# Kernel optimization log

Measured on AMD Instinct MI355X. Metric: run time of the kernel, lower is better.

Reference implementation:

```python
import math
import jax, jax.numpy as jnp
import numpy as np

NQ = 10      # n_qubits
NB = 4       # n_blocks (angle encoding layers)
VD = 6       # vqc_depth (hardware-efficient layers)
LAT = 128    # latent_dim
NOBS = 9     # n_qubits - k_local + 1 sliding 2-local groups
DIM = 2 ** NQ


def sin_embed(t, dim):
    half = dim // 2
    freqs = jnp.exp(-math.log(10000.0) * jnp.arange(half, dtype=jnp.float32) / half)
    args = t[:, None] * freqs[None, :]
    return jnp.concatenate([jnp.cos(args), jnp.sin(args)], axis=-1)


def apply_ry(psi, theta, q):
    # psi: [B, 2^NQ] complex; theta: scalar or [B]
    B = psi.shape[0]
    p = psi.reshape(B, 2 ** q, 2, 2 ** (NQ - 1 - q))
    th = jnp.broadcast_to(theta, (B,))
    c = jnp.cos(th / 2)[:, None, None].astype(psi.dtype)
    s = jnp.sin(th / 2)[:, None, None].astype(psi.dtype)
    p0, p1 = p[:, :, 0, :], p[:, :, 1, :]
    return jnp.stack([c * p0 - s * p1, s * p0 + c * p1], axis=2).reshape(B, -1)


def apply_cnot(psi, ctrl, tgt):
    B = psi.shape[0]
    pt = psi.reshape((B,) + (2,) * NQ)
    p0 = jax.lax.index_in_dim(pt, 0, axis=ctrl + 1, keepdims=True)
    p1 = jnp.flip(jax.lax.index_in_dim(pt, 1, axis=ctrl + 1, keepdims=True), axis=tgt + 1)
    return jnp.concatenate([p0, p1], axis=ctrl + 1).reshape(B, -1)


def run_circuit(enc, var_params):
    B = enc.shape[0]
    psi = jnp.zeros((B, DIM), dtype=jnp.complex64).at[:, 0].set(1.0)
    # angle encoding: RY data re-uploading blocks with CNOT ladders between blocks
    for layer in range(NB):
        for q in range(NQ):
            psi = apply_ry(psi, enc[:, layer * NQ + q], q)
        if layer < NB - 1:
            for q in range(0, NQ - 1, 2):
                psi = apply_cnot(psi, q, q + 1)
            for q in range(1, NQ - 1, 2):
                psi = apply_cnot(psi, q, q + 1)
    # hardware-efficient variational layers
    for ly in range(VD):
        for q in range(NQ):
            psi = apply_ry(psi, var_params[ly, q], q)
        for q in range(0, NQ - 1, 2):
            psi = apply_cnot(psi, q, q + 1)
        for q in range(1, NQ - 1, 2):
            psi = apply_cnot(psi, q, q + 1)
    return psi


def build_H(A_p, B_p, D_p):
    # create_Hermitian: lower-tri (row-major) = A + iB; h[i-1,i-1] = D[i]; H = h + h^dagger
    r, c = np.tril_indices(4, -1)  # order matches count+j loop: (1,0),(2,0),(2,1),(3,0),(3,1),(3,2)
    L = jnp.zeros((NOBS, 4, 4), dtype=jnp.complex64)
    L = L.at[:, r, c].set(A_p.astype(jnp.complex64) + 1j * B_p.astype(jnp.complex64))
    d = 2.0 * jnp.concatenate([D_p[:, 1:4], jnp.zeros((NOBS, 1), dtype=D_p.dtype)], axis=1)
    H = L + jnp.conj(jnp.swapaxes(L, 1, 2))
    H = H + jax.vmap(jnp.diag)(d).astype(jnp.complex64)
    return H


def expvals(psi, H):
    B = psi.shape[0]
    outs = []
    for s in range(NOBS):  # sliding window [s, s+1]
        pg = psi.reshape(B, 2 ** s, 4, 2 ** (NQ - s - 2))
        outs.append(jnp.einsum('balr,lk,bakr->b', jnp.conj(pg), H[s], pg).real)
    return jnp.stack(outs, axis=-1)


def setup_inputs() -> dict:
    ks = jax.random.split(jax.random.key(0), 12)
    B = 2048
    return {
        'z_t': jax.random.normal(ks[0], (B, LAT), dtype=jnp.float32),
        't': jax.random.uniform(ks[1], (B,), dtype=jnp.float32),
        'W1': 0.05 * jax.random.normal(ks[2], (2 * LAT, 256), dtype=jnp.float32),
        'b1': jnp.zeros((256,), dtype=jnp.float32),
        'W2': 0.05 * jax.random.normal(ks[3], (256, NB * NQ), dtype=jnp.float32),
        'b2': jnp.zeros((NB * NQ,), dtype=jnp.float32),
        'var_params': 0.01 * jax.random.normal(ks[4], (VD, NQ), dtype=jnp.float32),
        'A_p': 2.0 * jax.random.normal(ks[5], (NOBS, 6), dtype=jnp.float32),
        'B_p': 2.0 * jax.random.normal(ks[6], (NOBS, 6), dtype=jnp.float32),
        'D_p': 2.0 * jax.random.normal(ks[7], (NOBS, 4), dtype=jnp.float32),
        'W3': 0.05 * jax.random.normal(ks[8], (NOBS, 256), dtype=jnp.float32),
        'b3': jnp.zeros((256,), dtype=jnp.float32),
        'W4': 0.05 * jax.random.normal(ks[9], (256, LAT), dtype=jnp.float32),
        'b4': jnp.zeros((LAT,), dtype=jnp.float32),
    }


def reference(z_t, t, W1, b1, W2, b2, var_params, A_p, B_p, D_p, W3, b3, W4, b4):
    x = jnp.concatenate([z_t, sin_embed(t, LAT)], axis=-1)   # [B, 2*LAT]
    h = jax.nn.silu(x @ W1 + b1)
    enc = h @ W2 + b2                                         # [B, NB*NQ]
    psi = run_circuit(enc, var_params)                        # [B, 2^NQ]
    obs = expvals(psi, build_H(A_p, B_p, D_p))                # [B, NOBS]
    return jax.nn.silu(obs @ W3 + b3) @ W4 + b4               # [B, LAT]
```

## Files before the change

### kernel.cpp

```cpp
#include <hip/hip_runtime.h>
#include <math.h>

#define NQ   10
#define DIM  1024
#define NOBS 9
#define LATD 128

__device__ __forceinline__ float silu_f(float x) { return x / (1.f + expf(-x)); }

template<int CTRL>
__device__ __forceinline__ float dpp_perm(float x) {
  return __int_as_float(__builtin_amdgcn_update_dpp(0, __float_as_int(x), CTRL, 0xF, 0xF, true));
}


__device__ __forceinline__ float wave_reduce_sum(float x) {
#pragma unroll
  for (int m = 32; m >= 1; m >>= 1) x += __shfl_xor(x, m, 64);
  return x;
}

template<int M>
__device__ __forceinline__ void ry_reg(float v[16], float c, float s) {
#pragma unroll
  for (int r = 0; r < 16; ++r) {
    if ((r & M) == 0) {
      float p0 = v[r], p1 = v[r | M];
      v[r]     = c * p0 - s * p1;
      v[r | M] = s * p0 + c * p1;
    }
  }
}

template<int MASK>
__device__ __forceinline__ void ry_lane(float v[16], float c, float s, int lane) {
  float sp = (lane & MASK) ? s : -s;
#pragma unroll
  for (int r = 0; r < 16; ++r) {
    float p = __shfl_xor(v[r], MASK, 64);
    v[r] = c * v[r] + sp * p;
  }
}

template<int CTRL, int MASK>
__device__ __forceinline__ void ry_lane_dpp(float v[16], float c, float s, int lane) {
  float sp = (lane & MASK) ? s : -s;
#pragma unroll
  for (int r = 0; r < 16; ++r) {
    float p = dpp_perm<CTRL>(v[r]);
    v[r] = c * v[r] + sp * p;
  }
}

__device__ __forceinline__ void apply_rys(float v[16], int lane,
                                          const float* __restrict__ cc,
                                          const float* __restrict__ ss) {
  ry_reg<8>(v, cc[0], ss[0]);
  ry_reg<4>(v, cc[1], ss[1]);
  ry_reg<2>(v, cc[2], ss[2]);
  ry_reg<1>(v, cc[3], ss[3]);
  ry_lane<32>(v, cc[4], ss[4], lane);
  ry_lane<16>(v, cc[5], ss[5], lane);
  ry_lane_dpp<0x128, 8>(v, cc[6], ss[6], lane);
  ry_lane<4>(v, cc[7], ss[7], lane);
  ry_lane_dpp<0x4E, 2>(v, cc[8], ss[8], lane);
  ry_lane_dpp<0xB1, 1>(v, cc[9], ss[9], lane);
}

__device__ __forceinline__ void cnot_ladder(float v[16], int lane) {
  float t;
  t=v[8];  v[8]=v[12];  v[12]=t;
  t=v[9];  v[9]=v[13];  v[13]=t;
  t=v[10]; v[10]=v[14]; v[14]=t;
  t=v[11]; v[11]=v[15]; v[15]=t;
  t=v[2];  v[2]=v[3];   v[3]=t;
  t=v[6];  v[6]=v[7];   v[7]=t;
  t=v[10]; v[10]=v[11]; v[11]=t;
  t=v[14]; v[14]=v[15]; v[15]=t;
  int se = lane ^ ((lane & 42) >> 1);
#pragma unroll
  for (int r = 0; r < 16; ++r) v[r] = __shfl(v[r], se, 64);
  t=v[4];  v[4]=v[6];   v[6]=t;
  t=v[5];  v[5]=v[7];   v[7]=t;
  t=v[12]; v[12]=v[14]; v[14]=t;
  t=v[13]; v[13]=v[15]; v[15]=t;
  int so  = lane ^ ((lane & 20) >> 1);
  int so1 = so ^ 32;
#pragma unroll
  for (int r = 0; r < 16; ++r) v[r] = __shfl(v[r], (r & 1) ? so1 : so, 64);
}


__global__ __launch_bounds__(64) void varcs_kernel(const float* __restrict__ varp,
                                                   float* __restrict__ varc,
                                                   float* __restrict__ vars) {
  int tid = threadIdx.x;
  if (tid < 60) {
    float s, c;
    sincosf(0.5f * varp[tid], &s, &c);
    varc[tid] = c;
    vars[tid] = s;
  }
}

__global__ __launch_bounds__(256) void enc_kernel(
    const float* __restrict__ z, const float* __restrict__ t,
    const float* __restrict__ W1, const float* __restrict__ b1,
    const float* __restrict__ W2, const float* __restrict__ b2,
    float* __restrict__ encc, float* __restrict__ encs) {
  __shared__ float xs[4][256];
  __shared__ float hs[4][256];
  int tid = threadIdx.x;
  int b0 = blockIdx.x * 4;
#pragma unroll
  for (int r = 0; r < 4; ++r) {
    int b = b0 + r;
    if (tid < 128) {
      xs[r][tid] = z[b * 128 + tid];
    } else {
      int i = tid - 128, j = i & 63;
      float freq = expf(-9.2103403719761836f * (float)j * (1.f / 64.f));
      float arg = t[b] * freq;
      xs[r][tid] = (i < 64) ? cosf(arg) : sinf(arg);
    }
  }
  __syncthreads();
  float bv = b1[tid];
  float a0 = bv, a1 = bv, a2 = bv, a3 = bv;
  for (int k = 0; k < 256; k += 4) {
    float w0 = W1[(k + 0) * 256 + tid];
    float w1 = W1[(k + 1) * 256 + tid];
    float w2 = W1[(k + 2) * 256 + tid];
    float w3 = W1[(k + 3) * 256 + tid];
    float4 x0 = *(const float4*)&xs[0][k];
    float4 x1 = *(const float4*)&xs[1][k];
    float4 x2 = *(const float4*)&xs[2][k];
    float4 x3 = *(const float4*)&xs[3][k];
    a0 = fmaf(x0.w, w3, fmaf(x0.z, w2, fmaf(x0.y, w1, fmaf(x0.x, w0, a0))));
    a1 = fmaf(x1.w, w3, fmaf(x1.z, w2, fmaf(x1.y, w1, fmaf(x1.x, w0, a1))));
    a2 = fmaf(x2.w, w3, fmaf(x2.z, w2, fmaf(x2.y, w1, fmaf(x2.x, w0, a2))));
    a3 = fmaf(x3.w, w3, fmaf(x3.z, w2, fmaf(x3.y, w1, fmaf(x3.x, w0, a3))));
  }
  hs[0][tid] = silu_f(a0);
  hs[1][tid] = silu_f(a1);
  hs[2][tid] = silu_f(a2);
  hs[3][tid] = silu_f(a3);
  __syncthreads();
  if (tid < 160) {
    int r = tid / 40, c = tid - r * 40;
    float acc = b2[c];
    for (int k = 0; k < 256; k += 4) {
      float4 h = *(const float4*)&hs[r][k];
      acc = fmaf(h.x, W2[(k + 0) * 40 + c], acc);
      acc = fmaf(h.y, W2[(k + 1) * 40 + c], acc);
      acc = fmaf(h.z, W2[(k + 2) * 40 + c], acc);
      acc = fmaf(h.w, W2[(k + 3) * 40 + c], acc);
    }
    int b = b0 + r;
    float s, cv;
    sincosf(0.5f * acc, &s, &cv);
    encc[b * 40 + c] = cv;
    encs[b * 40 + c] = s;
  }
}

__global__ __launch_bounds__(64) void circuit_kernel(
    const float* __restrict__ encc, const float* __restrict__ encs,
    const float* __restrict__ varc, const float* __restrict__ vars,
    const float* __restrict__ A_p, const float* __restrict__ D_p,
    float* __restrict__ obs) {
  __shared__ float sw[DIM];
  int lane = threadIdx.x;
  int b = blockIdx.x;
  const float* cc = encc + b * 40;
  const float* ss = encs + b * 40;

  float base = 1.f;
  base *= (lane & 32) ? ss[4] : cc[4];
  base *= (lane & 16) ? ss[5] : cc[5];
  base *= (lane & 8)  ? ss[6] : cc[6];
  base *= (lane & 4)  ? ss[7] : cc[7];
  base *= (lane & 2)  ? ss[8] : cc[8];
  base *= (lane & 1)  ? ss[9] : cc[9];
  float v[16];
#pragma unroll
  for (int r = 0; r < 16; ++r) {
    float p = base;
    p *= (r & 8) ? ss[0] : cc[0];
    p *= (r & 4) ? ss[1] : cc[1];
    p *= (r & 2) ? ss[2] : cc[2];
    p *= (r & 1) ? ss[3] : cc[3];
    v[r] = p;
  }
  cnot_ladder(v, lane);
#pragma unroll 1
  for (int layer = 1; layer < 4; ++layer) {
    apply_rys(v, lane, cc + layer * 10, ss + layer * 10);
    if (layer < 3) cnot_ladder(v, lane);
  }
#pragma unroll 1
  for (int ly = 0; ly < 6; ++ly) {
    apply_rys(v, lane, varc + ly * 10, vars + ly * 10);
    cnot_ladder(v, lane);
  }

#pragma unroll
  for (int r = 0; r < 16; ++r) sw[r * 64 + lane] = v[r];

#pragma unroll
  for (int s = 0; s < NOBS; ++s) {
    const int r8 = 8 - s;
    const int stride = 1 << r8;
    float h10 = A_p[s*6+0], h20 = A_p[s*6+1], h21 = A_p[s*6+2];
    float h30 = A_p[s*6+3], h31 = A_p[s*6+4], h32 = A_p[s*6+5];
    float d0 = 2.f * D_p[s*4+1], d1 = 2.f * D_p[s*4+2], d2 = 2.f * D_p[s*4+3];
    float acc = 0.f;
#pragma unroll
    for (int k = 0; k < 4; ++k) {
      int p = lane + 64 * k;
      int a  = p >> r8;
      int rr = p & (stride - 1);
      int bse = (a << (r8 + 2)) + rr;
      float x0 = sw[bse];
      float x1 = sw[bse + stride];
      float x2 = sw[bse + 2 * stride];
      float x3 = sw[bse + 3 * stride];
      acc += d0 * x0 * x0 + d1 * x1 * x1 + d2 * x2 * x2
           + 2.f * (h10 * x1 * x0 + h20 * x2 * x0 + h21 * x2 * x1
                  + h30 * x3 * x0 + h31 * x3 * x1 + h32 * x3 * x2);
    }
    acc = wave_reduce_sum(acc);
    if (lane == 0) obs[b * NOBS + s] = acc;
  }
}

__global__ __launch_bounds__(256) void head_kernel(
    const float* __restrict__ obs, const float* __restrict__ W3,
    const float* __restrict__ b3, const float* __restrict__ W4,
    const float* __restrict__ b4, float* __restrict__ out) {
  __shared__ float os[4][NOBS];
  __shared__ float hs[4][256];
  int tid = threadIdx.x;
  int b0 = blockIdx.x * 4;
  if (tid < 4 * NOBS) os[tid / NOBS][tid % NOBS] = obs[b0 * NOBS + tid];
  __syncthreads();
  float bv = b3[tid];
  float a0 = bv, a1 = bv, a2 = bv, a3 = bv;
#pragma unroll
  for (int s = 0; s < NOBS; ++s) {
    float w = W3[s * 256 + tid];
    a0 = fmaf(os[0][s], w, a0);
    a1 = fmaf(os[1][s], w, a1);
    a2 = fmaf(os[2][s], w, a2);
    a3 = fmaf(os[3][s], w, a3);
  }
  hs[0][tid] = silu_f(a0);
  hs[1][tid] = silu_f(a1);
  hs[2][tid] = silu_f(a2);
  hs[3][tid] = silu_f(a3);
  __syncthreads();
  int c = tid & 127, rg = tid >> 7;
  const float* h0 = hs[rg * 2];
  const float* h1 = hs[rg * 2 + 1];
  float o0 = b4[c], o1 = b4[c];
  for (int k = 0; k < 256; k += 4) {
    float w0 = W4[(k + 0) * 128 + c];
    float w1 = W4[(k + 1) * 128 + c];
    float w2 = W4[(k + 2) * 128 + c];
    float w3 = W4[(k + 3) * 128 + c];
    float4 ha = *(const float4*)&h0[k];
    float4 hb = *(const float4*)&h1[k];
    o0 = fmaf(ha.w, w3, fmaf(ha.z, w2, fmaf(ha.y, w1, fmaf(ha.x, w0, o0))));
    o1 = fmaf(hb.w, w3, fmaf(hb.z, w2, fmaf(hb.y, w1, fmaf(hb.x, w0, o1))));
  }
  out[(b0 + rg * 2) * LATD + c]     = o0;
  out[(b0 + rg * 2 + 1) * LATD + c] = o1;
}


extern "C" void kernel_launch(void* const* d_in, const int* in_sizes, int n_in,
                              void* d_out, int out_size, void* d_ws, size_t ws_size,
                              hipStream_t stream) {
  const float* z_t  = (const float*)d_in[0];
  const float* t    = (const float*)d_in[1];
  const float* W1   = (const float*)d_in[2];
  const float* b1   = (const float*)d_in[3];
  const float* W2   = (const float*)d_in[4];
  const float* b2   = (const float*)d_in[5];
  const float* varp = (const float*)d_in[6];
  const float* A_p  = (const float*)d_in[7];
  const float* D_p  = (const float*)d_in[9];
  const float* W3   = (const float*)d_in[10];
  const float* b3   = (const float*)d_in[11];
  const float* W4   = (const float*)d_in[12];
  const float* b4   = (const float*)d_in[13];
  float* out = (float*)d_out;

  int B = in_sizes[1];

  float* encc = (float*)d_ws;
  float* encs = encc + (size_t)B * 40;
  float* obs  = encs + (size_t)B * 40;
  float* varc = obs  + (size_t)B * 9;
  float* vars = varc + 64;

  varcs_kernel<<<1, 64, 0, stream>>>(varp, varc, vars);
  enc_kernel<<<B / 4, 256, 0, stream>>>(z_t, t, W1, b1, W2, b2, encc, encs);
  circuit_kernel<<<B, 64, 0, stream>>>(encc, encs, varc, vars, A_p, D_p, obs);
  head_kernel<<<B / 4, 256, 0, stream>>>(obs, W3, b3, W4, b4, out);
}
```

Measured before the change: 132.1 us.

## Fuse encoder, circuit and head into one kernel with cheaper cross-lane permutes

Merges the four kernels (var angle sincos, encoder MLP, statevector circuit, head MLP) into a single 256-thread block that handles four batch rows, one wave per row for the circuit. Intermediates now live in shared memory instead of global workspace, which removes three launches and the global round trips. The generic __shfl lane exchanges in the RY gates, CNOT ladders and the reduction are replaced with DPP, ds_swizzle and permlane32/16 swaps, with fallbacks when those builtins are missing. The cost is higher LDS use per block (about 25 KB) and the sincos of the variational angles being recomputed in every block.

```diff
diff --git a/kernel.cpp b/kernel.cpp
--- a/kernel.cpp
+++ b/kernel.cpp
@@ -1,24 +1,67 @@
 #include <hip/hip_runtime.h>
 #include <math.h>
 
-#define NQ   10
-#define DIM  1024
 #define NOBS 9
 #define LATD 128
 
+typedef unsigned u32x2 __attribute__((ext_vector_type(2)));
+
 __device__ __forceinline__ float silu_f(float x) { return x / (1.f + expf(-x)); }
+
 
 template<int CTRL>
 __device__ __forceinline__ float dpp_perm(float x) {
   return __int_as_float(__builtin_amdgcn_update_dpp(0, __float_as_int(x), CTRL, 0xF, 0xF, true));
 }
-
-
-__device__ __forceinline__ float wave_reduce_sum(float x) {
-#pragma unroll
-  for (int m = 32; m >= 1; m >>= 1) x += __shfl_xor(x, m, 64);
+template<int PAT>
+__device__ __forceinline__ float ds_swz(float x) {
+  return __int_as_float(__builtin_amdgcn_ds_swizzle(__float_as_int(x), PAT));
+}
+
+__device__ __forceinline__ float x4(float x) { return ds_swz<0x101F>(x); }
+
+#if __has_builtin(__builtin_amdgcn_permlane32_swap)
+#define PL32 1
+__device__ __forceinline__ float x32(float x, bool sel) {
+  u32x2 r = __builtin_amdgcn_permlane32_swap(__float_as_uint(x), __float_as_uint(x), false, false);
+  return __uint_as_float(sel ? r.x : r.y);
+}
+__device__ __forceinline__ float sum32(float x) {
+  u32x2 r = __builtin_amdgcn_permlane32_swap(__float_as_uint(x), __float_as_uint(x), false, false);
+  return __uint_as_float(r.x) + __uint_as_float(r.y);
+}
+#else
+#define PL32 0
+__device__ __forceinline__ float x32(float x, bool sel) { return __shfl_xor(x, 32, 64); }
+__device__ __forceinline__ float sum32(float x) { return x + __shfl_xor(x, 32, 64); }
+#endif
+
+#if __has_builtin(__builtin_amdgcn_permlane16_swap)
+#define PL16 1
+__device__ __forceinline__ float x16(float x, bool sel) {
+  u32x2 r = __builtin_amdgcn_permlane16_swap(__float_as_uint(x), __float_as_uint(x), false, false);
+  return __uint_as_float(sel ? r.x : r.y);
+}
+__device__ __forceinline__ float sum16(float x) {
+  u32x2 r = __builtin_amdgcn_permlane16_swap(__float_as_uint(x), __float_as_uint(x), false, false);
+  return __uint_as_float(r.x) + __uint_as_float(r.y);
+}
+#else
+#define PL16 0
+__device__ __forceinline__ float x16(float x, bool sel) { return ds_swz<0x401F>(x); }
+__device__ __forceinline__ float sum16(float x) { return x + ds_swz<0x401F>(x); }
+#endif
+
+__device__ __forceinline__ float wave_sum(float x) {
+  x += dpp_perm<0xB1>(x);
+  x += dpp_perm<0x4E>(x);
+  x += x4(x);
+  x += dpp_perm<0x128>(x);
+  x = sum16(x);
+  x = sum32(x);
   return x;
 }
+
 
 template<int M>
 __device__ __forceinline__ void ry_reg(float v[16], float c, float s) {
@@ -32,42 +75,34 @@
   }
 }
 
-template<int MASK>
-__device__ __forceinline__ void ry_lane(float v[16], float c, float s, int lane) {
-  float sp = (lane & MASK) ? s : -s;
-#pragma unroll
-  for (int r = 0; r < 16; ++r) {
-    float p = __shfl_xor(v[r], MASK, 64);
-    v[r] = c * v[r] + sp * p;
-  }
-}
-
-template<int CTRL, int MASK>
-__device__ __forceinline__ void ry_lane_dpp(float v[16], float c, float s, int lane) {
-  float sp = (lane & MASK) ? s : -s;
-#pragma unroll
-  for (int r = 0; r < 16; ++r) {
-    float p = dpp_perm<CTRL>(v[r]);
-    v[r] = c * v[r] + sp * p;
-  }
-}
-
-__device__ __forceinline__ void apply_rys(float v[16], int lane,
+__device__ __forceinline__ void apply_rys(float v[16], int lane, bool sel32, bool sel16,
                                           const float* __restrict__ cc,
                                           const float* __restrict__ ss) {
   ry_reg<8>(v, cc[0], ss[0]);
   ry_reg<4>(v, cc[1], ss[1]);
   ry_reg<2>(v, cc[2], ss[2]);
   ry_reg<1>(v, cc[3], ss[3]);
-  ry_lane<32>(v, cc[4], ss[4], lane);
-  ry_lane<16>(v, cc[5], ss[5], lane);
-  ry_lane_dpp<0x128, 8>(v, cc[6], ss[6], lane);
-  ry_lane<4>(v, cc[7], ss[7], lane);
-  ry_lane_dpp<0x4E, 2>(v, cc[8], ss[8], lane);
-  ry_lane_dpp<0xB1, 1>(v, cc[9], ss[9], lane);
-}
-
-__device__ __forceinline__ void cnot_ladder(float v[16], int lane) {
+  { float c = cc[4], s = ss[4], sp = (lane & 32) ? s : -s;
+#pragma unroll
+    for (int r = 0; r < 16; ++r) { float p = x32(v[r], sel32); v[r] = fmaf(c, v[r], sp * p); } }
+  { float c = cc[5], s = ss[5], sp = (lane & 16) ? s : -s;
+#pragma unroll
+    for (int r = 0; r < 16; ++r) { float p = x16(v[r], sel16); v[r] = fmaf(c, v[r], sp * p); } }
+  { float c = cc[6], s = ss[6], sp = (lane & 8) ? s : -s;
+#pragma unroll
+    for (int r = 0; r < 16; ++r) { float p = dpp_perm<0x128>(v[r]); v[r] = fmaf(c, v[r], sp * p); } }
+  { float c = cc[7], s = ss[7], sp = (lane & 4) ? s : -s;
+#pragma unroll
+    for (int r = 0; r < 16; ++r) { float p = x4(v[r]); v[r] = fmaf(c, v[r], sp * p); } }
+  { float c = cc[8], s = ss[8], sp = (lane & 2) ? s : -s;
+#pragma unroll
+    for (int r = 0; r < 16; ++r) { float p = dpp_perm<0x4E>(v[r]); v[r] = fmaf(c, v[r], sp * p); } }
+  { float c = cc[9], s = ss[9], sp = (lane & 1) ? s : -s;
+#pragma unroll
+    for (int r = 0; r < 16; ++r) { float p = dpp_perm<0xB1>(v[r]); v[r] = fmaf(c, v[r], sp * p); } }
+}
+
+__device__ __forceinline__ void cnot_ladder(float v[16], int lane, bool sel32, bool sel16) {
   float t;
   t=v[8];  v[8]=v[12];  v[12]=t;
   t=v[9];  v[9]=v[13];  v[13]=t;
@@ -77,41 +112,55 @@
   t=v[6];  v[6]=v[7];   v[7]=t;
   t=v[10]; v[10]=v[11]; v[11]=t;
   t=v[14]; v[14]=v[15]; v[15]=t;
-  int se = lane ^ ((lane & 42) >> 1);
-#pragma unroll
-  for (int r = 0; r < 16; ++r) v[r] = __shfl(v[r], se, 64);
+  { bool c45 = (lane & 32);
+#pragma unroll
+    for (int r = 0; r < 16; ++r) { float p = x16(v[r], sel16); v[r] = c45 ? p : v[r]; } }
+  { bool c67 = (lane & 8);
+#pragma unroll
+    for (int r = 0; r < 16; ++r) { float p = x4(v[r]); v[r] = c67 ? p : v[r]; } }
+  { bool c89 = (lane & 2);
+#pragma unroll
+    for (int r = 0; r < 16; ++r) { float p = dpp_perm<0xB1>(v[r]); v[r] = c89 ? p : v[r]; } }
   t=v[4];  v[4]=v[6];   v[6]=t;
   t=v[5];  v[5]=v[7];   v[7]=t;
   t=v[12]; v[12]=v[14]; v[14]=t;
   t=v[13]; v[13]=v[15]; v[15]=t;
-  int so  = lane ^ ((lane & 20) >> 1);
-  int so1 = so ^ 32;
-#pragma unroll
-  for (int r = 0; r < 16; ++r) v[r] = __shfl(v[r], (r & 1) ? so1 : so, 64);
-}
-
-
-__global__ __launch_bounds__(64) void varcs_kernel(const float* __restrict__ varp,
-                                                   float* __restrict__ varc,
-                                                   float* __restrict__ vars) {
+#pragma unroll
+  for (int r = 1; r < 16; r += 2) v[r] = x32(v[r], sel32);
+  { bool c56 = (lane & 16);
+#pragma unroll
+    for (int r = 0; r < 16; ++r) { float p = dpp_perm<0x128>(v[r]); v[r] = c56 ? p : v[r]; } }
+  { bool c78 = (lane & 4);
+#pragma unroll
+    for (int r = 0; r < 16; ++r) { float p = dpp_perm<0x4E>(v[r]); v[r] = c78 ? p : v[r]; } }
+}
+
+
+__global__ __launch_bounds__(256) void fused_kernel(
+    const float* __restrict__ z, const float* __restrict__ t,
+    const float* __restrict__ W1, const float* __restrict__ b1,
+    const float* __restrict__ W2, const float* __restrict__ b2,
+    const float* __restrict__ varp,
+    const float* __restrict__ A_p, const float* __restrict__ D_p,
+    const float* __restrict__ W3, const float* __restrict__ b3,
+    const float* __restrict__ W4, const float* __restrict__ b4,
+    float* __restrict__ out) {
+  __shared__ float xs[4][256];
+  __shared__ float hs[4][256];
+  __shared__ float dump[4][1024];
+  __shared__ float cs[4][40], sn[4][40];
+  __shared__ float vcs[60], vsn[60];
+  __shared__ float os[4][NOBS];
+
   int tid = threadIdx.x;
+  int b0 = blockIdx.x * 4;
+
   if (tid < 60) {
     float s, c;
     sincosf(0.5f * varp[tid], &s, &c);
-    varc[tid] = c;
-    vars[tid] = s;
-  }
-}
-
-__global__ __launch_bounds__(256) void enc_kernel(
-    const float* __restrict__ z, const float* __restrict__ t,
-    const float* __restrict__ W1, const float* __restrict__ b1,
-    const float* __restrict__ W2, const float* __restrict__ b2,
-    float* __restrict__ encc, float* __restrict__ encs) {
-  __shared__ float xs[4][256];
-  __shared__ float hs[4][256];
-  int tid = threadIdx.x;
-  int b0 = blockIdx.x * 4;
+    vcs[tid] = c; vsn[tid] = s;
+  }
+
 #pragma unroll
   for (int r = 0; r < 4; ++r) {
     int b = b0 + r;
@@ -125,30 +174,36 @@
     }
   }
   __syncthreads();
-  float bv = b1[tid];
-  float a0 = bv, a1 = bv, a2 = bv, a3 = bv;
-  for (int k = 0; k < 256; k += 4) {
-    float w0 = W1[(k + 0) * 256 + tid];
-    float w1 = W1[(k + 1) * 256 + tid];
-    float w2 = W1[(k + 2) * 256 + tid];
-    float w3 = W1[(k + 3) * 256 + tid];
-    float4 x0 = *(const float4*)&xs[0][k];
-    float4 x1 = *(const float4*)&xs[1][k];
-    float4 x2 = *(const float4*)&xs[2][k];
-    float4 x3 = *(const float4*)&xs[3][k];
-    a0 = fmaf(x0.w, w3, fmaf(x0.z, w2, fmaf(x0.y, w1, fmaf(x0.x, w0, a0))));
-    a1 = fmaf(x1.w, w3, fmaf(x1.z, w2, fmaf(x1.y, w1, fmaf(x1.x, w0, a1))));
-    a2 = fmaf(x2.w, w3, fmaf(x2.z, w2, fmaf(x2.y, w1, fmaf(x2.x, w0, a2))));
-    a3 = fmaf(x3.w, w3, fmaf(x3.z, w2, fmaf(x3.y, w1, fmaf(x3.x, w0, a3))));
-  }
-  hs[0][tid] = silu_f(a0);
-  hs[1][tid] = silu_f(a1);
-  hs[2][tid] = silu_f(a2);
-  hs[3][tid] = silu_f(a3);
-  __syncthreads();
+
+  {
+    float bv = b1[tid];
+    float a0 = bv, a1 = bv, a2 = bv, a3 = bv;
+#pragma unroll 4
+    for (int k = 0; k < 256; k += 4) {
+      float w0 = W1[(k + 0) * 256 + tid];
+      float w1 = W1[(k + 1) * 256 + tid];
+      float w2 = W1[(k + 2) * 256 + tid];
+      float w3 = W1[(k + 3) * 256 + tid];
+      float4 x0 = *(const float4*)&xs[0][k];
+      float4 x1 = *(const float4*)&xs[1][k];
+      float4 x2 = *(const float4*)&xs[2][k];
+      float4 x3 = *(const float4*)&xs[3][k];
+      a0 = fmaf(x0.w, w3, fmaf(x0.z, w2, fmaf(x0.y, w1, fmaf(x0.x, w0, a0))));
+      a1 = fmaf(x1.w, w3, fmaf(x1.z, w2, fmaf(x1.y, w1, fmaf(x1.x, w0, a1))));
+      a2 = fmaf(x2.w, w3, fmaf(x2.z, w2, fmaf(x2.y, w1, fmaf(x2.x, w0, a2))));
+      a3 = fmaf(x3.w, w3, fmaf(x3.z, w2, fmaf(x3.y, w1, fmaf(x3.x, w0, a3))));
+    }
+    hs[0][tid] = silu_f(a0);
+    hs[1][tid] = silu_f(a1);
+    hs[2][tid] = silu_f(a2);
+    hs[3][tid] = silu_f(a3);
+  }
+  __syncthreads();
+
   if (tid < 160) {
     int r = tid / 40, c = tid - r * 40;
     float acc = b2[c];
+#pragma unroll 4
     for (int k = 0; k < 256; k += 4) {
       float4 h = *(const float4*)&hs[r][k];
       acc = fmaf(h.x, W2[(k + 0) * 40 + c], acc);
@@ -156,125 +211,124 @@
       acc = fmaf(h.z, W2[(k + 2) * 40 + c], acc);
       acc = fmaf(h.w, W2[(k + 3) * 40 + c], acc);
     }
-    int b = b0 + r;
     float s, cv;
     sincosf(0.5f * acc, &s, &cv);
-    encc[b * 40 + c] = cv;
-    encs[b * 40 + c] = s;
-  }
-}
-
-__global__ __launch_bounds__(64) void circuit_kernel(
-    const float* __restrict__ encc, const float* __restrict__ encs,
-    const float* __restrict__ varc, const float* __restrict__ vars,
-    const float* __restrict__ A_p, const float* __restrict__ D_p,
-    float* __restrict__ obs) {
-  __shared__ float sw[DIM];
-  int lane = threadIdx.x;
-  int b = blockIdx.x;
-  const float* cc = encc + b * 40;
-  const float* ss = encs + b * 40;
-
-  float base = 1.f;
-  base *= (lane & 32) ? ss[4] : cc[4];
-  base *= (lane & 16) ? ss[5] : cc[5];
-  base *= (lane & 8)  ? ss[6] : cc[6];
-  base *= (lane & 4)  ? ss[7] : cc[7];
-  base *= (lane & 2)  ? ss[8] : cc[8];
-  base *= (lane & 1)  ? ss[9] : cc[9];
-  float v[16];
-#pragma unroll
-  for (int r = 0; r < 16; ++r) {
-    float p = base;
-    p *= (r & 8) ? ss[0] : cc[0];
-    p *= (r & 4) ? ss[1] : cc[1];
-    p *= (r & 2) ? ss[2] : cc[2];
-    p *= (r & 1) ? ss[3] : cc[3];
-    v[r] = p;
-  }
-  cnot_ladder(v, lane);
+    cs[r][c] = cv; sn[r][c] = s;
+  }
+  __syncthreads();
+
+  {
+    int wave = tid >> 6;
+    int lane = tid & 63;
+    bool sel32 = true, sel16 = true;
+#if PL32
+    { u32x2 tt = __builtin_amdgcn_permlane32_swap((unsigned)lane, (unsigned)lane, false, false);
+      sel32 = (tt.x == (unsigned)(lane ^ 32)); }
+#endif
+#if PL16
+    { u32x2 tt = __builtin_amdgcn_permlane16_swap((unsigned)lane, (unsigned)lane, false, false);
+      sel16 = (tt.x == (unsigned)(lane ^ 16)); }
+#endif
+    const float* cc = cs[wave];
+    const float* ss = sn[wave];
+
+    float base = 1.f;
+    base *= (lane & 32) ? ss[4] : cc[4];
+    base *= (lane & 16) ? ss[5] : cc[5];
+    base *= (lane & 8)  ? ss[6] : cc[6];
+    base *= (lane & 4)  ? ss[7] : cc[7];
+    base *= (lane & 2)  ? ss[8] : cc[8];
+    base *= (lane & 1)  ? ss[9] : cc[9];
+    float v[16];
+#pragma unroll
+    for (int r = 0; r < 16; ++r) {
+      float p = base;
+      p *= (r & 8) ? ss[0] : cc[0];
+      p *= (r & 4) ? ss[1] : cc[1];
+      p *= (r & 2) ? ss[2] : cc[2];
+      p *= (r & 1) ? ss[3] : cc[3];
+      v[r] = p;
+    }
+    cnot_ladder(v, lane, sel32, sel16);
 #pragma unroll 1
-  for (int layer = 1; layer < 4; ++layer) {
-    apply_rys(v, lane, cc + layer * 10, ss + layer * 10);
-    if (layer < 3) cnot_ladder(v, lane);
-  }
+    for (int layer = 1; layer < 4; ++layer) {
+      apply_rys(v, lane, sel32, sel16, cc + layer * 10, ss + layer * 10);
+      if (layer < 3) cnot_ladder(v, lane, sel32, sel16);
+    }
 #pragma unroll 1
-  for (int ly = 0; ly < 6; ++ly) {
-    apply_rys(v, lane, varc + ly * 10, vars + ly * 10);
-    cnot_ladder(v, lane);
-  }
-
-#pragma unroll
-  for (int r = 0; r < 16; ++r) sw[r * 64 + lane] = v[r];
-
-#pragma unroll
-  for (int s = 0; s < NOBS; ++s) {
-    const int r8 = 8 - s;
-    const int stride = 1 << r8;
-    float h10 = A_p[s*6+0], h20 = A_p[s*6+1], h21 = A_p[s*6+2];
-    float h30 = A_p[s*6+3], h31 = A_p[s*6+4], h32 = A_p[s*6+5];
-    float d0 = 2.f * D_p[s*4+1], d1 = 2.f * D_p[s*4+2], d2 = 2.f * D_p[s*4+3];
-    float acc = 0.f;
-#pragma unroll
-    for (int k = 0; k < 4; ++k) {
-      int p = lane + 64 * k;
-      int a  = p >> r8;
-      int rr = p & (stride - 1);
-      int bse = (a << (r8 + 2)) + rr;
-      float x0 = sw[bse];
-      float x1 = sw[bse + stride];
-      float x2 = sw[bse + 2 * stride];
-      float x3 = sw[bse + 3 * stride];
-      acc += d0 * x0 * x0 + d1 * x1 * x1 + d2 * x2 * x2
-           + 2.f * (h10 * x1 * x0 + h20 * x2 * x0 + h21 * x2 * x1
-                  + h30 * x3 * x0 + h31 * x3 * x1 + h32 * x3 * x2);
-    }
-    acc = wave_reduce_sum(acc);
-    if (lane == 0) obs[b * NOBS + s] = acc;
-  }
-}
-
-__global__ __launch_bounds__(256) void head_kernel(
-    const float* __restrict__ obs, const float* __restrict__ W3,
-    const float* __restrict__ b3, const float* __restrict__ W4,
-    const float* __restrict__ b4, float* __restrict__ out) {
-  __shared__ float os[4][NOBS];
-  __shared__ float hs[4][256];
-  int tid = threadIdx.x;
-  int b0 = blockIdx.x * 4;
-  if (tid < 4 * NOBS) os[tid / NOBS][tid % NOBS] = obs[b0 * NOBS + tid];
-  __syncthreads();
-  float bv = b3[tid];
-  float a0 = bv, a1 = bv, a2 = bv, a3 = bv;
-#pragma unroll
-  for (int s = 0; s < NOBS; ++s) {
-    float w = W3[s * 256 + tid];
-    a0 = fmaf(os[0][s], w, a0);
-    a1 = fmaf(os[1][s], w, a1);
-    a2 = fmaf(os[2][s], w, a2);
-    a3 = fmaf(os[3][s], w, a3);
-  }
-  hs[0][tid] = silu_f(a0);
-  hs[1][tid] = silu_f(a1);
-  hs[2][tid] = silu_f(a2);
-  hs[3][tid] = silu_f(a3);
-  __syncthreads();
-  int c = tid & 127, rg = tid >> 7;
-  const float* h0 = hs[rg * 2];
-  const float* h1 = hs[rg * 2 + 1];
-  float o0 = b4[c], o1 = b4[c];
-  for (int k = 0; k < 256; k += 4) {
-    float w0 = W4[(k + 0) * 128 + c];
-    float w1 = W4[(k + 1) * 128 + c];
-    float w2 = W4[(k + 2) * 128 + c];
-    float w3 = W4[(k + 3) * 128 + c];
-    float4 ha = *(const float4*)&h0[k];
-    float4 hb = *(const float4*)&h1[k];
-    o0 = fmaf(ha.w, w3, fmaf(ha.z, w2, fmaf(ha.y, w1, fmaf(ha.x, w0, o0))));
-    o1 = fmaf(hb.w, w3, fmaf(hb.z, w2, fmaf(hb.y, w1, fmaf(hb.x, w0, o1))));
-  }
-  out[(b0 + rg * 2) * LATD + c]     = o0;
-  out[(b0 + rg * 2 + 1) * LATD + c] = o1;
+    for (int ly = 0; ly < 6; ++ly) {
+      apply_rys(v, lane, sel32, sel16, vcs + ly * 10, vsn + ly * 10);
+      cnot_ladder(v, lane, sel32, sel16);
+    }
+
+    float* sw = dump[wave];
+#pragma unroll
+    for (int r = 0; r < 16; ++r) sw[r * 64 + lane] = v[r];
+
+#pragma unroll 1
+    for (int s = 0; s < NOBS; ++s) {
+      const int r8 = 8 - s;
+      const int stride = 1 << r8;
+      float h10 = A_p[s*6+0], h20 = A_p[s*6+1], h21 = A_p[s*6+2];
+      float h30 = A_p[s*6+3], h31 = A_p[s*6+4], h32 = A_p[s*6+5];
+      float d0 = 2.f * D_p[s*4+1], d1 = 2.f * D_p[s*4+2], d2 = 2.f * D_p[s*4+3];
+      float acc = 0.f;
+#pragma unroll
+      for (int k = 0; k < 4; ++k) {
+        int p = lane + 64 * k;
+        int a  = p >> r8;
+        int rr = p & (stride - 1);
+        int bse = (a << (r8 + 2)) + rr;
+        float x0 = sw[bse];
+        float x1 = sw[bse + stride];
+        float x2 = sw[bse + 2 * stride];
+        float x3 = sw[bse + 3 * stride];
+        acc += d0 * x0 * x0 + d1 * x1 * x1 + d2 * x2 * x2
+             + 2.f * (h10 * x1 * x0 + h20 * x2 * x0 + h21 * x2 * x1
+                    + h30 * x3 * x0 + h31 * x3 * x1 + h32 * x3 * x2);
+      }
+      acc = wave_sum(acc);
+      if (lane == 0) os[wave][s] = acc;
+    }
+  }
+  __syncthreads();
+
+  {
+    float bv = b3[tid];
+    float a0 = bv, a1 = bv, a2 = bv, a3 = bv;
+#pragma unroll
+    for (int s = 0; s < NOBS; ++s) {
+      float w = W3[s * 256 + tid];
+      a0 = fmaf(os[0][s], w, a0);
+      a1 = fmaf(os[1][s], w, a1);
+      a2 = fmaf(os[2][s], w, a2);
+      a3 = fmaf(os[3][s], w, a3);
+    }
+    hs[0][tid] = silu_f(a0);
+    hs[1][tid] = silu_f(a1);
+    hs[2][tid] = silu_f(a2);
+    hs[3][tid] = silu_f(a3);
+  }
+  __syncthreads();
+  {
+    int c = tid & 127, rg = tid >> 7;
+    const float* h0 = hs[rg * 2];
+    const float* h1 = hs[rg * 2 + 1];
+    float o0 = b4[c], o1 = b4[c];
+#pragma unroll 4
+    for (int k = 0; k < 256; k += 4) {
+      float w0 = W4[(k + 0) * 128 + c];
+      float w1 = W4[(k + 1) * 128 + c];
+      float w2 = W4[(k + 2) * 128 + c];
+      float w3 = W4[(k + 3) * 128 + c];
+      float4 ha = *(const float4*)&h0[k];
+      float4 hb = *(const float4*)&h1[k];
+      o0 = fmaf(ha.w, w3, fmaf(ha.z, w2, fmaf(ha.y, w1, fmaf(ha.x, w0, o0))));
+      o1 = fmaf(hb.w, w3, fmaf(hb.z, w2, fmaf(hb.y, w1, fmaf(hb.x, w0, o1))));
+    }
+    out[(b0 + rg * 2) * LATD + c]     = o0;
+    out[(b0 + rg * 2 + 1) * LATD + c] = o1;
+  }
 }
 
 
@@ -298,14 +352,6 @@
 
   int B = in_sizes[1];
 
-  float* encc = (float*)d_ws;
-  float* encs = encc + (size_t)B * 40;
-  float* obs  = encs + (size_t)B * 40;
-  float* varc = obs  + (size_t)B * 9;
-  float* vars = varc + 64;
-
-  varcs_kernel<<<1, 64, 0, stream>>>(varp, varc, vars);
-  enc_kernel<<<B / 4, 256, 0, stream>>>(z_t, t, W1, b1, W2, b2, encc, encs);
-  circuit_kernel<<<B, 64, 0, stream>>>(encc, encs, varc, vars, A_p, D_p, obs);
-  head_kernel<<<B / 4, 256, 0, stream>>>(obs, W3, b3, W4, b4, out);
-}
+  fused_kernel<<<B / 4, 256, 0, stream>>>(z_t, t, W1, b1, W2, b2, varp,
+                                          A_p, D_p, W3, b3, W4, b4, out);
+}
```

New measurement: 128.8 us. 2.5% less time.
